# Kernel optimization log

Measured on AMD Instinct MI355X. Metric: run time of the kernel, lower is better.

## Reference

```python
import jax, jax.numpy as jnp
import numpy as np

B, L, D = 2, 2048, 1024
DH = 64
NH = D // DH
EPS = 1e-5
NEG = -1e30


def rms_norm(x, w):
    # x: (..., dh); norm in fp32 like the torch module, then scale by weight
    xf = x.astype(jnp.float32)
    y = xf * jax.lax.rsqrt(jnp.mean(xf * xf, axis=-1, keepdims=True) + EPS)
    return y.astype(x.dtype) * w.astype(x.dtype)


def sdpa(q, k, v, m):
    # q:(b,h,lq,dh) k,v:(b,h,lk,dh) m:(lq,lk) bool
    scale = 1.0 / jnp.sqrt(jnp.asarray(DH, q.dtype))
    s = jnp.einsum('bhqd,bhkd->bhqk', q, k) * scale
    s = jnp.where(m[None, None], s, NEG)
    p = jax.nn.softmax(s, axis=-1)
    return jnp.einsum('bhqk,bhkd->bhqd', p, v)


def setup_inputs() -> dict:
    key = jax.random.key(0)
    k1, k2, k3 = jax.random.split(key, 3)
    x = jax.random.normal(k1, (B, L, D), dtype=jnp.float32)
    mask = jnp.tril(jnp.ones((L, L), dtype=bool))  # causal: no fully-masked rows
    w_qkv = jax.random.normal(k2, (3 * D, D), dtype=jnp.float32) * (1.0 / np.sqrt(D))
    w_fc = jax.random.normal(k3, (D, D), dtype=jnp.float32) * (1.0 / np.sqrt(D))
    q_norm_w = jnp.ones((DH,), dtype=jnp.float32)
    k_norm_w = jnp.ones((DH,), dtype=jnp.float32)
    return {"x": x, "mask": mask, "w_qkv": w_qkv, "w_fc": w_fc,
            "q_norm_w": q_norm_w, "k_norm_w": k_norm_w,
            "subset_attention_size": 1024}


def reference(x, mask, w_qkv, w_fc, q_norm_w, k_norm_w, subset_attention_size):
    b, l, d = x.shape
    qkv = jnp.einsum('bld,ed->ble', x, w_qkv)  # (b,l,3d)
    q, k, v = jnp.split(qkv, 3, axis=-1)

    def heads(t):
        return t.reshape(b, l, NH, DH).transpose(0, 2, 1, 3)  # (b,nh,l,dh)

    q, k, v = heads(q), heads(k), heads(v)
    q = rms_norm(q, q_norm_w)
    k = rms_norm(k, k_norm_w)

    S = subset_attention_size
    if S is not None and S < l:
        o1 = sdpa(q[:, :, :S], k[:, :, :S], v[:, :, :S], mask[:S, :S])
        o2 = sdpa(q[:, :, S:], k, v, mask[S:, :])
        o = jnp.concatenate([o1, o2], axis=2)
    else:
        o = sdpa(q, k, v, mask)
    o = o.transpose(0, 2, 1, 3).reshape(b, l, d)  # (b,l,d)
    return jnp.einsum('bld,ed->ble', o, w_fc)
```

## Files before the change

kernel.cpp:

```cpp
#include <hip/hip_runtime.h>

typedef __bf16 bf16x8 __attribute__((ext_vector_type(8)));
typedef __bf16 bf16x4 __attribute__((ext_vector_type(4)));
typedef float f32x4 __attribute__((ext_vector_type(4)));
typedef unsigned short u16;
typedef unsigned int u32;
typedef unsigned short u16x4 __attribute__((ext_vector_type(4)));
typedef unsigned short u16x8 __attribute__((ext_vector_type(8)));

#define AS1 __attribute__((address_space(1)))
#define AS3 __attribute__((address_space(3)))

__device__ __forceinline__ u16 f2bf(float f) {
  unsigned u = __builtin_bit_cast(unsigned, f);
  u += 0x7fffu + ((u >> 16) & 1u);
  return (u16)(u >> 16);
}

__global__ __launch_bounds__(256) void cvt_all(const float* __restrict__ x,
                                               const float* __restrict__ wq,
                                               const float* __restrict__ wf,
                                               u16* __restrict__ xb, u16* __restrict__ wqb,
                                               u16* __restrict__ wfb) {
  long i = ((long)blockIdx.x * 256 + threadIdx.x) * 4;
  const float* src;
  u16* dst;
  long off;
  if (i < 4194304L) {
    src = x; dst = xb; off = i;
  } else if (i < 7340032L) {
    src = wq; dst = wqb; off = i - 4194304L;
  } else {
    src = wf; dst = wfb; off = i - 7340032L;
  }
  float4 v = *reinterpret_cast<const float4*>(src + off);
  u16x4 o;
  o.x = f2bf(v.x); o.y = f2bf(v.y); o.z = f2bf(v.z); o.w = f2bf(v.w);
  *reinterpret_cast<u16x4*>(dst + off) = o;
}

__global__ __launch_bounds__(256, 2) void gemm_qkv(const u16* __restrict__ A,
                                                   const u16* __restrict__ W,
                                                   u16* __restrict__ C,
                                                   const float* __restrict__ qw,
                                                   const float* __restrict__ kw) {
  constexpr int N = 3072, K = 1024;
  __shared__ __align__(16) u16 As[128 * 32];
  __shared__ __align__(16) u16 Bs[128 * 32];
  const int tid = threadIdx.x;
  const int lane = tid & 63;
  const int wid = tid >> 6;
  const int wm = wid >> 1, wn = wid & 1;
  const int l16 = lane & 15, g4 = lane >> 4;
  const long bm = blockIdx.x, bn = blockIdx.y;

  const int srow = tid >> 2;
  const int scol = (tid & 3) * 8;
  const u16* aA0 = A + (bm * 128 + srow) * (long)K + scol;
  const u16* aA1 = aA0 + 64 * (long)K;
  const u16* aW0 = W + (bn * 128 + srow) * (long)K + scol;
  const u16* aW1 = aW0 + 64 * (long)K;

  f32x4 acc[4][4] = {};

  for (int kt = 0; kt < K; kt += 32) {
    __builtin_amdgcn_global_load_lds((AS1 void*)(aA0 + kt), (AS3 void*)(&As[tid * 8]), 16, 0, 0);
    __builtin_amdgcn_global_load_lds((AS1 void*)(aA1 + kt), (AS3 void*)(&As[2048 + tid * 8]), 16, 0, 0);
    __builtin_amdgcn_global_load_lds((AS1 void*)(aW0 + kt), (AS3 void*)(&Bs[tid * 8]), 16, 0, 0);
    __builtin_amdgcn_global_load_lds((AS1 void*)(aW1 + kt), (AS3 void*)(&Bs[2048 + tid * 8]), 16, 0, 0);
    __syncthreads();
    bf16x8 af[4], bfr[4];
#pragma unroll
    for (int m = 0; m < 4; ++m)
      af[m] = *reinterpret_cast<const bf16x8*>(&As[(wm * 64 + m * 16 + l16) * 32 + g4 * 8]);
#pragma unroll
    for (int n = 0; n < 4; ++n)
      bfr[n] = *reinterpret_cast<const bf16x8*>(&Bs[(wn * 64 + n * 16 + l16) * 32 + g4 * 8]);
#pragma unroll
    for (int m = 0; m < 4; ++m)
#pragma unroll
      for (int n = 0; n < 4; ++n)
        acc[m][n] = __builtin_amdgcn_mfma_f32_16x16x32_bf16(af[m], bfr[n], acc[m][n], 0, 0, 0);
    __syncthreads();
  }

  if (bn < 16) {
    const float* w = (bn < 8) ? qw : kw;
    float wv[4];
#pragma unroll
    for (int n = 0; n < 4; ++n) wv[n] = w[n * 16 + l16];
#pragma unroll
    for (int m = 0; m < 4; ++m) {
#pragma unroll
      for (int j = 0; j < 4; ++j) {
        float ss = 0.f;
#pragma unroll
        for (int n = 0; n < 4; ++n) ss = fmaf(acc[m][n][j], acc[m][n][j], ss);
        ss += __shfl_xor(ss, 1);
        ss += __shfl_xor(ss, 2);
        ss += __shfl_xor(ss, 4);
        ss += __shfl_xor(ss, 8);
        const float inv = rsqrtf(ss * (1.0f / 64.0f) + 1e-5f);
#pragma unroll
        for (int n = 0; n < 4; ++n) acc[m][n][j] *= inv * wv[n];
      }
    }
  }

#pragma unroll
  for (int m = 0; m < 4; ++m)
#pragma unroll
    for (int n = 0; n < 4; ++n)
#pragma unroll
      for (int j = 0; j < 4; ++j) {
        long row = bm * 128 + wm * 64 + m * 16 + g4 * 4 + j;
        long col = bn * 128 + wn * 64 + n * 16 + l16;
        C[row * N + col] = f2bf(acc[m][n][j]);
      }
}

__global__ __launch_bounds__(256, 2) void gemm_fc(const u16* __restrict__ A,
                                                  const u16* __restrict__ W,
                                                  float* __restrict__ C) {
  constexpr int N = 1024, K = 1024;
  __shared__ __align__(16) u16 As[128 * 32];
  __shared__ __align__(16) u16 Bs[64 * 32];
  const int tid = threadIdx.x;
  const int lane = tid & 63;
  const int wid = tid >> 6;
  const int wm = wid >> 1, wn = wid & 1;
  const int l16 = lane & 15, g4 = lane >> 4;
  const long bm = blockIdx.x, bn = blockIdx.y;

  const int srow = tid >> 2;
  const int scol = (tid & 3) * 8;
  const u16* aA0 = A + (bm * 128 + srow) * (long)K + scol;
  const u16* aA1 = aA0 + 64 * (long)K;
  const u16* aW0 = W + (bn * 64 + srow) * (long)K + scol;

  f32x4 acc[4][2] = {};

  for (int kt = 0; kt < K; kt += 32) {
    __builtin_amdgcn_global_load_lds((AS1 void*)(aA0 + kt), (AS3 void*)(&As[tid * 8]), 16, 0, 0);
    __builtin_amdgcn_global_load_lds((AS1 void*)(aA1 + kt), (AS3 void*)(&As[2048 + tid * 8]), 16, 0, 0);
    __builtin_amdgcn_global_load_lds((AS1 void*)(aW0 + kt), (AS3 void*)(&Bs[tid * 8]), 16, 0, 0);
    __syncthreads();
    bf16x8 af[4], bfr[2];
#pragma unroll
    for (int m = 0; m < 4; ++m)
      af[m] = *reinterpret_cast<const bf16x8*>(&As[(wm * 64 + m * 16 + l16) * 32 + g4 * 8]);
#pragma unroll
    for (int n = 0; n < 2; ++n)
      bfr[n] = *reinterpret_cast<const bf16x8*>(&Bs[(wn * 32 + n * 16 + l16) * 32 + g4 * 8]);
#pragma unroll
    for (int m = 0; m < 4; ++m)
#pragma unroll
      for (int n = 0; n < 2; ++n)
        acc[m][n] = __builtin_amdgcn_mfma_f32_16x16x32_bf16(af[m], bfr[n], acc[m][n], 0, 0, 0);
    __syncthreads();
  }

#pragma unroll
  for (int m = 0; m < 4; ++m)
#pragma unroll
    for (int n = 0; n < 2; ++n)
#pragma unroll
      for (int j = 0; j < 4; ++j) {
        long row = bm * 128 + wm * 64 + m * 16 + g4 * 4 + j;
        long col = bn * 64 + wn * 32 + n * 16 + l16;
        C[row * N + col] = acc[m][n][j];
      }
}

__global__ __launch_bounds__(256) void vtrans(const u16* __restrict__ qkv,
                                              u16* __restrict__ vt) {
  __shared__ u16 T[64][66];
  const int tid = threadIdx.x;
  const int f = blockIdx.x;
  const int bh = (f & 7) * 4 + (f >> 8);
  const int ktile = (f >> 3) & 31;
  const long vbase = (long)(bh >> 4) * 2048 * 3072 + (bh & 15) * 64 + 2048;
  const int r = tid >> 2, c = (tid & 3) * 16;
  const u16* src = qkv + vbase + (long)(ktile * 64 + r) * 3072 + c;
  *reinterpret_cast<u16x8*>(&T[r][c]) = *reinterpret_cast<const u16x8*>(src);
  *reinterpret_cast<u16x8*>(&T[r][c + 8]) = *reinterpret_cast<const u16x8*>(src + 8);
  __syncthreads();
  const int dr = tid >> 2, kc = (tid & 3) * 16;
  u16 buf[16];
#pragma unroll
  for (int j = 0; j < 16; ++j) buf[j] = T[kc + j][dr];
  u16* dst = vt + (long)bh * 131072 + (long)dr * 2048 + ktile * 64 + kc;
  *reinterpret_cast<u16x8*>(dst) = *reinterpret_cast<u16x8*>(&buf[0]);
  *reinterpret_cast<u16x8*>(dst + 8) = *reinterpret_cast<u16x8*>(&buf[8]);
}

__global__ __launch_bounds__(256, 2) void attn_causal(const u16* __restrict__ qkv,
                                                      const u16* __restrict__ vt,
                                                      u16* __restrict__ o) {
  __shared__ __align__(16) u16 Klds[2][4096];
  __shared__ __align__(16) u16 Vlds[2][4096];
  __shared__ __align__(16) u16 Plds[4][1024];

  const int tid = threadIdx.x, lane = tid & 63, wid = tid >> 6;
  const int l16 = lane & 15, g4 = lane >> 4;
  const int h8 = (l16 & 7) << 4;

  const int f = blockIdx.x;
  const int g = f >> 3;
  const int bh = (f & 7) * 4 + (g >> 4);
  const int i = g & 15;
  const int iA = i, iB = 31 - i;

  const long base = (long)(bh >> 4) * 2048 * 3072 + (bh & 15) * 64;
  const u16* qb = qkv + base;
  const u16* kb = qkv + base + 1024;
  const u16* vtb = vt + (long)bh * 131072;

  const u16* qpA = qb + ((long)iA * 64 + wid * 16 + l16) * 3072;
  const u16* qpB = qb + ((long)iB * 64 + wid * 16 + l16) * 3072;
  const bf16x8 qA0 = *reinterpret_cast<const bf16x8*>(qpA + g4 * 8);
  const bf16x8 qA1 = *reinterpret_cast<const bf16x8*>(qpA + 32 + g4 * 8);
  const bf16x8 qB0 = *reinterpret_cast<const bf16x8*>(qpB + g4 * 8);
  const bf16x8 qB1 = *reinterpret_cast<const bf16x8*>(qpB + 32 + g4 * 8);

  f32x4 accA[4] = {}, accB[4] = {};
  f32x4 laccA = {}, laccB = {};
  const float cl = 0.125f * 1.4426950408889634f;
  const float mc = -8.0f * cl;

  const int krow = tid >> 3;
  const int scolE = (((tid & 7) * 16) ^ ((krow & 7) << 4)) >> 1;

  auto stage_issue = [&](int buf, int kt) {
    __builtin_amdgcn_global_load_lds((AS1 void*)(kb + (long)(kt * 64 + krow) * 3072 + scolE),
                                     (AS3 void*)(&Klds[buf][tid * 8]), 16, 0, 0);
    __builtin_amdgcn_global_load_lds((AS1 void*)(kb + (long)(kt * 64 + krow + 32) * 3072 + scolE),
                                     (AS3 void*)(&Klds[buf][2048 + tid * 8]), 16, 0, 0);
    __builtin_amdgcn_global_load_lds((AS1 void*)(vtb + (long)krow * 2048 + kt * 64 + scolE),
                                     (AS3 void*)(&Vlds[buf][tid * 8]), 16, 0, 0);
    __builtin_amdgcn_global_load_lds((AS1 void*)(vtb + (long)(krow + 32) * 2048 + kt * 64 + scolE),
                                     (AS3 void*)(&Vlds[buf][2048 + tid * 8]), 16, 0, 0);
  };

  auto tile_step = [&](f32x4* acc, f32x4& lacc, const bf16x8& q0, const bf16x8& q1, bool diag,
                       bf16x8 (&kf)[4][2], bf16x8 (&vf)[4][2]) {
    f32x4 s[4];
    __builtin_amdgcn_s_setprio(1);
#pragma unroll
    for (int kn = 0; kn < 4; ++kn) {
      f32x4 z = {0.f, 0.f, 0.f, 0.f};
      z = __builtin_amdgcn_mfma_f32_16x16x32_bf16(kf[kn][0], q0, z, 0, 0, 0);
      z = __builtin_amdgcn_mfma_f32_16x16x32_bf16(kf[kn][1], q1, z, 0, 0, 0);
      s[kn] = z;
    }
    __builtin_amdgcn_s_setprio(0);
    if (diag) {
      const int qrel = wid * 16 + l16;
#pragma unroll
      for (int kn = 0; kn < 4; ++kn)
#pragma unroll
        for (int j = 0; j < 4; ++j)
          if (kn * 16 + g4 * 4 + j > qrel) s[kn][j] = -3e38f;
    }
#pragma unroll
    for (int kn = 0; kn < 4; ++kn) {
#pragma unroll
      for (int j = 0; j < 4; ++j) s[kn][j] = exp2f(fmaf(s[kn][j], cl, mc));
      lacc += s[kn];
    }
    u16* pl = &Plds[wid][0];
#pragma unroll
    for (int kn = 0; kn < 4; ++kn) {
      bf16x4 w4;
      w4[0] = (__bf16)s[kn][0];
      w4[1] = (__bf16)s[kn][1];
      w4[2] = (__bf16)s[kn][2];
      w4[3] = (__bf16)s[kn][3];
      const int boff = (kn * 32 + g4 * 8) ^ h8;
      *reinterpret_cast<bf16x4*>(&pl[l16 * 64 + (boff >> 1)]) = w4;
    }
    const bf16x8 pa0 = *reinterpret_cast<const bf16x8*>(&pl[l16 * 64 + (((g4 * 16) ^ h8) >> 1)]);
    const bf16x8 pa1 =
        *reinterpret_cast<const bf16x8*>(&pl[l16 * 64 + (((64 + g4 * 16) ^ h8) >> 1)]);
    __builtin_amdgcn_s_setprio(1);
#pragma unroll
    for (int n = 0; n < 4; ++n) {
      acc[n] = __builtin_amdgcn_mfma_f32_16x16x32_bf16(pa0, vf[n][0], acc[n], 0, 0, 0);
      acc[n] = __builtin_amdgcn_mfma_f32_16x16x32_bf16(pa1, vf[n][1], acc[n], 0, 0, 0);
    }
    __builtin_amdgcn_s_setprio(0);
  };

  stage_issue(0, 0);
  __syncthreads();

  for (int kt = 0; kt <= iB; ++kt) {
    const int cur = kt & 1, nxt = cur ^ 1;
    if (kt < iB) stage_issue(nxt, kt + 1);

    bf16x8 kf[4][2], vf[4][2];
#pragma unroll
    for (int kn = 0; kn < 4; ++kn) {
      const int row = kn * 16 + l16;
#pragma unroll
      for (int ck = 0; ck < 2; ++ck) {
        const int boff = (ck * 64 + g4 * 16) ^ h8;
        kf[kn][ck] = *reinterpret_cast<const bf16x8*>(&Klds[cur][row * 64 + (boff >> 1)]);
        vf[kn][ck] = *reinterpret_cast<const bf16x8*>(&Vlds[cur][row * 64 + (boff >> 1)]);
      }
    }

    if (kt <= iA) tile_step(accA, laccA, qA0, qA1, kt == iA, kf, vf);
    tile_step(accB, laccB, qB0, qB1, kt == iB, kf, vf);

    __syncthreads();
  }

  const long obase = (long)(bh >> 4) * 2048 * 1024 + (bh & 15) * 64;
  auto epi = [&](f32x4* acc, const f32x4& lacc, int qt) {
    float l = lacc[0] + lacc[1] + lacc[2] + lacc[3];
    l += __shfl_xor(l, 16);
    l += __shfl_xor(l, 32);
    float lR[4];
#pragma unroll
    for (int j = 0; j < 4; ++j) lR[j] = __shfl(l, g4 * 4 + j, 16);
    u16* op = o + obase + ((long)qt * 64 + wid * 16 + g4 * 4) * 1024;
#pragma unroll
    for (int n = 0; n < 4; ++n)
#pragma unroll
      for (int j = 0; j < 4; ++j)
        op[j * 1024 + n * 16 + l16] = f2bf(acc[n][j] / lR[j]);
  };
  epi(accA, laccA, iA);
  epi(accB, laccB, iB);
}

extern "C" void kernel_launch(void* const* d_in, const int* in_sizes, int n_in,
                              void* d_out, int out_size, void* d_ws, size_t ws_size,
                              hipStream_t stream) {
  const float* x = (const float*)d_in[0];
  const float* w_qkv = (const float*)d_in[2];
  const float* w_fc = (const float*)d_in[3];
  const float* qw = (const float*)d_in[4];
  const float* kw = (const float*)d_in[5];
  float* out = (float*)d_out;

  char* ws = (char*)d_ws;
  u16* xb    = (u16*)(ws);
  u16* wqkvb = (u16*)(ws + (8L << 20));
  u16* wfcb  = (u16*)(ws + (14L << 20));
  u16* qkv   = (u16*)(ws + (16L << 20));
  u16* ob    = (u16*)(ws + (40L << 20));
  u16* vt    = xb;

  cvt_all<<<8192, 256, 0, stream>>>(x, w_qkv, w_fc, xb, wqkvb, wfcb);
  gemm_qkv<<<dim3(32, 24), 256, 0, stream>>>(xb, wqkvb, qkv, qw, kw);
  vtrans<<<1024, 256, 0, stream>>>(qkv, vt);
  attn_causal<<<512, 256, 0, stream>>>(qkv, vt, ob);
  gemm_fc<<<dim3(32, 16), 256, 0, stream>>>(ob, wfcb, out);
}
```

Measured before the change: 113.5 us.

## Stage 128-key tiles per barrier, fold softmax scale into Q norm, MFMA row sums

The attention kernel now loads K/V tiles of 128 keys per stage, processing two 64-key subtiles between barriers, which halves barrier and staging overhead per key. The softmax scale times log2(e) is folded into the Q RMS-norm weight, so the exp needs no fma. The fixed -8 max offset is dropped, which relies on normed q·k staying bounded. Row sums are computed with an MFMA against a ones vector instead of VALU adds and shuffles, and LDS use doubles, which may affect occupancy.

Result: no change. 113.1 us (-0.4%).

```diff
diff --git a/kernel.cpp b/kernel.cpp
--- a/kernel.cpp
+++ b/kernel.cpp
@@ -85,10 +85,12 @@
   }
 
   if (bn < 16) {
+    const float qscale = 0.18033688011112042f;
     const float* w = (bn < 8) ? qw : kw;
+    const float ws = (bn < 8) ? qscale : 1.0f;
     float wv[4];
 #pragma unroll
-    for (int n = 0; n < 4; ++n) wv[n] = w[n * 16 + l16];
+    for (int n = 0; n < 4; ++n) wv[n] = w[n * 16 + l16] * ws;
 #pragma unroll
     for (int m = 0; m < 4; ++m) {
 #pragma unroll
@@ -197,8 +199,8 @@
 __global__ __launch_bounds__(256, 2) void attn_causal(const u16* __restrict__ qkv,
                                                       const u16* __restrict__ vt,
                                                       u16* __restrict__ o) {
-  __shared__ __align__(16) u16 Klds[2][4096];
-  __shared__ __align__(16) u16 Vlds[2][4096];
+  __shared__ __align__(16) u16 Klds[2][8192];
+  __shared__ __align__(16) u16 Vlds[2][8192];
   __shared__ __align__(16) u16 Plds[4][1024];
 
   const int tid = threadIdx.x, lane = tid & 63, wid = tid >> 6;
@@ -225,21 +227,27 @@
 
   f32x4 accA[4] = {}, accB[4] = {};
   f32x4 laccA = {}, laccB = {};
-  const float cl = 0.125f * 1.4426950408889634f;
-  const float mc = -8.0f * cl;
+
+  bf16x8 ones;
+#pragma unroll
+  for (int j = 0; j < 8; ++j) ones[j] = (__bf16)1.0f;
 
   const int krow = tid >> 3;
   const int scolE = (((tid & 7) * 16) ^ ((krow & 7) << 4)) >> 1;
+  const int vrow = tid >> 4;
+  const int vcolE = (((tid & 15) * 16) ^ ((vrow & 7) << 4)) >> 1;
 
   auto stage_issue = [&](int buf, int kt) {
-    __builtin_amdgcn_global_load_lds((AS1 void*)(kb + (long)(kt * 64 + krow) * 3072 + scolE),
-                                     (AS3 void*)(&Klds[buf][tid * 8]), 16, 0, 0);
-    __builtin_amdgcn_global_load_lds((AS1 void*)(kb + (long)(kt * 64 + krow + 32) * 3072 + scolE),
-                                     (AS3 void*)(&Klds[buf][2048 + tid * 8]), 16, 0, 0);
-    __builtin_amdgcn_global_load_lds((AS1 void*)(vtb + (long)krow * 2048 + kt * 64 + scolE),
-                                     (AS3 void*)(&Vlds[buf][tid * 8]), 16, 0, 0);
-    __builtin_amdgcn_global_load_lds((AS1 void*)(vtb + (long)(krow + 32) * 2048 + kt * 64 + scolE),
-                                     (AS3 void*)(&Vlds[buf][2048 + tid * 8]), 16, 0, 0);
+    const u16* ks = kb + (long)(kt * 128 + krow) * 3072 + scolE;
+#pragma unroll
+    for (int c = 0; c < 4; ++c)
+      __builtin_amdgcn_global_load_lds((AS1 void*)(ks + (long)(32 * c) * 3072),
+                                       (AS3 void*)(&Klds[buf][c * 2048 + tid * 8]), 16, 0, 0);
+    const u16* vs = vtb + (long)vrow * 2048 + kt * 128 + vcolE;
+#pragma unroll
+    for (int c = 0; c < 4; ++c)
+      __builtin_amdgcn_global_load_lds((AS1 void*)(vs + (long)(16 * c) * 2048),
+                                       (AS3 void*)(&Vlds[buf][c * 2048 + tid * 8]), 16, 0, 0);
   };
 
   auto tile_step = [&](f32x4* acc, f32x4& lacc, const bf16x8& q0, const bf16x8& q1, bool diag,
@@ -263,11 +271,9 @@
           if (kn * 16 + g4 * 4 + j > qrel) s[kn][j] = -3e38f;
     }
 #pragma unroll
-    for (int kn = 0; kn < 4; ++kn) {
-#pragma unroll
-      for (int j = 0; j < 4; ++j) s[kn][j] = exp2f(fmaf(s[kn][j], cl, mc));
-      lacc += s[kn];
-    }
+    for (int kn = 0; kn < 4; ++kn)
+#pragma unroll
+      for (int j = 0; j < 4; ++j) s[kn][j] = exp2f(s[kn][j]);
     u16* pl = &Plds[wid][0];
 #pragma unroll
     for (int kn = 0; kn < 4; ++kn) {
@@ -283,6 +289,8 @@
     const bf16x8 pa1 =
         *reinterpret_cast<const bf16x8*>(&pl[l16 * 64 + (((64 + g4 * 16) ^ h8) >> 1)]);
     __builtin_amdgcn_s_setprio(1);
+    lacc = __builtin_amdgcn_mfma_f32_16x16x32_bf16(pa0, ones, lacc, 0, 0, 0);
+    lacc = __builtin_amdgcn_mfma_f32_16x16x32_bf16(pa1, ones, lacc, 0, 0, 0);
 #pragma unroll
     for (int n = 0; n < 4; ++n) {
       acc[n] = __builtin_amdgcn_mfma_f32_16x16x32_bf16(pa0, vf[n][0], acc[n], 0, 0, 0);
@@ -294,42 +302,44 @@
   stage_issue(0, 0);
   __syncthreads();
 
-  for (int kt = 0; kt <= iB; ++kt) {
+  const int ktmax = (iB + 2) >> 1;
+  for (int kt = 0; kt < ktmax; ++kt) {
     const int cur = kt & 1, nxt = cur ^ 1;
-    if (kt < iB) stage_issue(nxt, kt + 1);
-
-    bf16x8 kf[4][2], vf[4][2];
-#pragma unroll
-    for (int kn = 0; kn < 4; ++kn) {
-      const int row = kn * 16 + l16;
-#pragma unroll
-      for (int ck = 0; ck < 2; ++ck) {
-        const int boff = (ck * 64 + g4 * 16) ^ h8;
-        kf[kn][ck] = *reinterpret_cast<const bf16x8*>(&Klds[cur][row * 64 + (boff >> 1)]);
-        vf[kn][ck] = *reinterpret_cast<const bf16x8*>(&Vlds[cur][row * 64 + (boff >> 1)]);
+    if (kt + 1 < ktmax) stage_issue(nxt, kt + 1);
+
+#pragma unroll
+    for (int sub = 0; sub < 2; ++sub) {
+      const int kt2 = kt * 2 + sub;
+      if (kt2 > iB) break;
+
+      bf16x8 kf[4][2], vf[4][2];
+#pragma unroll
+      for (int kn = 0; kn < 4; ++kn) {
+        const int krowf = sub * 64 + kn * 16 + l16;
+        const int vrowf = kn * 16 + l16;
+#pragma unroll
+        for (int ck = 0; ck < 2; ++ck) {
+          const int kboff = (ck * 64 + g4 * 16) ^ h8;
+          kf[kn][ck] = *reinterpret_cast<const bf16x8*>(&Klds[cur][krowf * 64 + (kboff >> 1)]);
+          const int vboff = (sub * 128 + ck * 64 + g4 * 16) ^ h8;
+          vf[kn][ck] = *reinterpret_cast<const bf16x8*>(&Vlds[cur][vrowf * 128 + (vboff >> 1)]);
+        }
       }
-    }
-
-    if (kt <= iA) tile_step(accA, laccA, qA0, qA1, kt == iA, kf, vf);
-    tile_step(accB, laccB, qB0, qB1, kt == iB, kf, vf);
-
+
+      if (kt2 <= iA) tile_step(accA, laccA, qA0, qA1, kt2 == iA, kf, vf);
+      tile_step(accB, laccB, qB0, qB1, kt2 == iB, kf, vf);
+    }
     __syncthreads();
   }
 
   const long obase = (long)(bh >> 4) * 2048 * 1024 + (bh & 15) * 64;
   auto epi = [&](f32x4* acc, const f32x4& lacc, int qt) {
-    float l = lacc[0] + lacc[1] + lacc[2] + lacc[3];
-    l += __shfl_xor(l, 16);
-    l += __shfl_xor(l, 32);
-    float lR[4];
-#pragma unroll
-    for (int j = 0; j < 4; ++j) lR[j] = __shfl(l, g4 * 4 + j, 16);
     u16* op = o + obase + ((long)qt * 64 + wid * 16 + g4 * 4) * 1024;
 #pragma unroll
     for (int n = 0; n < 4; ++n)
 #pragma unroll
       for (int j = 0; j < 4; ++j)
-        op[j * 1024 + n * 16 + l16] = f2bf(acc[n][j] / lR[j]);
+        op[j * 1024 + n * 16 + l16] = f2bf(acc[n][j] / lacc[j]);
   };
   epi(accA, laccA, iA);
   epi(accB, laccB, iB);
```

## Split paired attention tiles into one-tile blocks; fold softmax scale into Q norm

Applied to the files above, without the earlier changes.

Each attention block previously handled a pair of query tiles (i, 31-i) sharing K/V loads. Now each block handles one query tile, launched as 1024 blocks with a balanced interleaved ordering, and launch bounds are raised to allow four blocks per CU. The softmax scale (1/8·log2e) is folded into the Q RMS-norm weights so exp2 takes the raw score, and the row sums are computed with an MFMA against a ones vector instead of VALU adds and shuffles. This trades K/V reuse across paired tiles for more parallelism and occupancy, and drops the fixed max offset while relying on bounded normalized scores.

After: 111.4 us. About the same (-1.9%).

```diff
diff --git a/kernel.cpp b/kernel.cpp
--- a/kernel.cpp
+++ b/kernel.cpp
@@ -85,10 +85,12 @@
   }
 
   if (bn < 16) {
+    const float qscale = 0.18033688011112042f;
     const float* w = (bn < 8) ? qw : kw;
+    const float ws = (bn < 8) ? qscale : 1.0f;
     float wv[4];
 #pragma unroll
-    for (int n = 0; n < 4; ++n) wv[n] = w[n * 16 + l16];
+    for (int n = 0; n < 4; ++n) wv[n] = w[n * 16 + l16] * ws;
 #pragma unroll
     for (int m = 0; m < 4; ++m) {
 #pragma unroll
@@ -194,7 +196,7 @@
   *reinterpret_cast<u16x8*>(dst + 8) = *reinterpret_cast<u16x8*>(&buf[8]);
 }
 
-__global__ __launch_bounds__(256, 2) void attn_causal(const u16* __restrict__ qkv,
+__global__ __launch_bounds__(256, 4) void attn_causal(const u16* __restrict__ qkv,
                                                       const u16* __restrict__ vt,
                                                       u16* __restrict__ o) {
   __shared__ __align__(16) u16 Klds[2][4096];
@@ -206,27 +208,29 @@
   const int h8 = (l16 & 7) << 4;
 
   const int f = blockIdx.x;
+  const int xcd = f & 7;
   const int g = f >> 3;
-  const int bh = (f & 7) * 4 + (g >> 4);
-  const int i = g & 15;
-  const int iA = i, iB = 31 - i;
+  const int hb = g >> 5;
+  const int w = g & 31;
+  const int bh = xcd * 4 + hb;
+  const int basei = (w & 1) ? (31 - (w >> 1)) : (w >> 1);
+  const int it = (hb & 1) ? (31 - basei) : basei;
 
   const long base = (long)(bh >> 4) * 2048 * 3072 + (bh & 15) * 64;
   const u16* qb = qkv + base;
   const u16* kb = qkv + base + 1024;
   const u16* vtb = vt + (long)bh * 131072;
 
-  const u16* qpA = qb + ((long)iA * 64 + wid * 16 + l16) * 3072;
-  const u16* qpB = qb + ((long)iB * 64 + wid * 16 + l16) * 3072;
-  const bf16x8 qA0 = *reinterpret_cast<const bf16x8*>(qpA + g4 * 8);
-  const bf16x8 qA1 = *reinterpret_cast<const bf16x8*>(qpA + 32 + g4 * 8);
-  const bf16x8 qB0 = *reinterpret_cast<const bf16x8*>(qpB + g4 * 8);
-  const bf16x8 qB1 = *reinterpret_cast<const bf16x8*>(qpB + 32 + g4 * 8);
-
-  f32x4 accA[4] = {}, accB[4] = {};
-  f32x4 laccA = {}, laccB = {};
-  const float cl = 0.125f * 1.4426950408889634f;
-  const float mc = -8.0f * cl;
+  const u16* qp = qb + ((long)it * 64 + wid * 16 + l16) * 3072;
+  const bf16x8 q0 = *reinterpret_cast<const bf16x8*>(qp + g4 * 8);
+  const bf16x8 q1 = *reinterpret_cast<const bf16x8*>(qp + 32 + g4 * 8);
+
+  f32x4 acc[4] = {};
+  f32x4 lacc = {};
+
+  bf16x8 ones;
+#pragma unroll
+  for (int j = 0; j < 8; ++j) ones[j] = (__bf16)1.0f;
 
   const int krow = tid >> 3;
   const int scolE = (((tid & 7) * 16) ^ ((krow & 7) << 4)) >> 1;
@@ -242,8 +246,16 @@
                                      (AS3 void*)(&Vlds[buf][2048 + tid * 8]), 16, 0, 0);
   };
 
-  auto tile_step = [&](f32x4* acc, f32x4& lacc, const bf16x8& q0, const bf16x8& q1, bool diag,
-                       bf16x8 (&kf)[4][2], bf16x8 (&vf)[4][2]) {
+  auto tile_step = [&](int cur, bool diag) {
+    bf16x8 kf[4][2];
+#pragma unroll
+    for (int kn = 0; kn < 4; ++kn) {
+      const int row = kn * 16 + l16;
+#pragma unroll
+      for (int ck = 0; ck < 2; ++ck)
+        kf[kn][ck] = *reinterpret_cast<const bf16x8*>(
+            &Klds[cur][row * 64 + (((ck * 64 + g4 * 16) ^ h8) >> 1)]);
+    }
     f32x4 s[4];
     __builtin_amdgcn_s_setprio(1);
 #pragma unroll
@@ -263,11 +275,9 @@
           if (kn * 16 + g4 * 4 + j > qrel) s[kn][j] = -3e38f;
     }
 #pragma unroll
-    for (int kn = 0; kn < 4; ++kn) {
-#pragma unroll
-      for (int j = 0; j < 4; ++j) s[kn][j] = exp2f(fmaf(s[kn][j], cl, mc));
-      lacc += s[kn];
-    }
+    for (int kn = 0; kn < 4; ++kn)
+#pragma unroll
+      for (int j = 0; j < 4; ++j) s[kn][j] = exp2f(s[kn][j]);
     u16* pl = &Plds[wid][0];
 #pragma unroll
     for (int kn = 0; kn < 4; ++kn) {
@@ -282,7 +292,18 @@
     const bf16x8 pa0 = *reinterpret_cast<const bf16x8*>(&pl[l16 * 64 + (((g4 * 16) ^ h8) >> 1)]);
     const bf16x8 pa1 =
         *reinterpret_cast<const bf16x8*>(&pl[l16 * 64 + (((64 + g4 * 16) ^ h8) >> 1)]);
+    bf16x8 vf[4][2];
+#pragma unroll
+    for (int n = 0; n < 4; ++n) {
+      const int row = n * 16 + l16;
+#pragma unroll
+      for (int ck = 0; ck < 2; ++ck)
+        vf[n][ck] = *reinterpret_cast<const bf16x8*>(
+            &Vlds[cur][row * 64 + (((ck * 64 + g4 * 16) ^ h8) >> 1)]);
+    }
     __builtin_amdgcn_s_setprio(1);
+    lacc = __builtin_amdgcn_mfma_f32_16x16x32_bf16(pa0, ones, lacc, 0, 0, 0);
+    lacc = __builtin_amdgcn_mfma_f32_16x16x32_bf16(pa1, ones, lacc, 0, 0, 0);
 #pragma unroll
     for (int n = 0; n < 4; ++n) {
       acc[n] = __builtin_amdgcn_mfma_f32_16x16x32_bf16(pa0, vf[n][0], acc[n], 0, 0, 0);
@@ -294,45 +315,21 @@
   stage_issue(0, 0);
   __syncthreads();
 
-  for (int kt = 0; kt <= iB; ++kt) {
-    const int cur = kt & 1, nxt = cur ^ 1;
-    if (kt < iB) stage_issue(nxt, kt + 1);
-
-    bf16x8 kf[4][2], vf[4][2];
-#pragma unroll
-    for (int kn = 0; kn < 4; ++kn) {
-      const int row = kn * 16 + l16;
-#pragma unroll
-      for (int ck = 0; ck < 2; ++ck) {
-        const int boff = (ck * 64 + g4 * 16) ^ h8;
-        kf[kn][ck] = *reinterpret_cast<const bf16x8*>(&Klds[cur][row * 64 + (boff >> 1)]);
-        vf[kn][ck] = *reinterpret_cast<const bf16x8*>(&Vlds[cur][row * 64 + (boff >> 1)]);
-      }
-    }
-
-    if (kt <= iA) tile_step(accA, laccA, qA0, qA1, kt == iA, kf, vf);
-    tile_step(accB, laccB, qB0, qB1, kt == iB, kf, vf);
-
-    __syncthreads();
-  }
+  for (int kt = 0; kt < it; ++kt) {
+    const int cur = kt & 1;
+    stage_issue(cur ^ 1, kt + 1);
+    tile_step(cur, false);
+    __syncthreads();
+  }
+  tile_step(it & 1, true);
 
   const long obase = (long)(bh >> 4) * 2048 * 1024 + (bh & 15) * 64;
-  auto epi = [&](f32x4* acc, const f32x4& lacc, int qt) {
-    float l = lacc[0] + lacc[1] + lacc[2] + lacc[3];
-    l += __shfl_xor(l, 16);
-    l += __shfl_xor(l, 32);
-    float lR[4];
-#pragma unroll
-    for (int j = 0; j < 4; ++j) lR[j] = __shfl(l, g4 * 4 + j, 16);
-    u16* op = o + obase + ((long)qt * 64 + wid * 16 + g4 * 4) * 1024;
-#pragma unroll
-    for (int n = 0; n < 4; ++n)
-#pragma unroll
-      for (int j = 0; j < 4; ++j)
-        op[j * 1024 + n * 16 + l16] = f2bf(acc[n][j] / lR[j]);
-  };
-  epi(accA, laccA, iA);
-  epi(accB, laccB, iB);
+  u16* op = o + obase + ((long)it * 64 + wid * 16 + g4 * 4) * 1024;
+#pragma unroll
+  for (int n = 0; n < 4; ++n)
+#pragma unroll
+    for (int j = 0; j < 4; ++j)
+      op[j * 1024 + n * 16 + l16] = f2bf(acc[n][j] / lacc[j]);
 }
 
 extern "C" void kernel_launch(void* const* d_in, const int* in_sizes, int n_in,
@@ -356,6 +353,6 @@
   cvt_all<<<8192, 256, 0, stream>>>(x, w_qkv, w_fc, xb, wqkvb, wfcb);
   gemm_qkv<<<dim3(32, 24), 256, 0, stream>>>(xb, wqkvb, qkv, qw, kw);
   vtrans<<<1024, 256, 0, stream>>>(qkv, vt);
-  attn_causal<<<512, 256, 0, stream>>>(qkv, vt, ob);
+  attn_causal<<<1024, 256, 0, stream>>>(qkv, vt, ob);
   gemm_fc<<<dim3(32, 16), 256, 0, stream>>>(ob, wfcb, out);
 }
```
